# Performance work log

Hardware: AMD Instinct MI355X
Metric: run time of the kernel (lower is better)

The kernel has to match this reference:

```python
import jax, jax.numpy as jnp
import numpy as np

B, H_IN, H_OUT, SEQ_LEN = 256, 512, 512, 512


def setup_inputs() -> dict:
    key = jax.random.key(0)
    k1, k2, k3, k4, k5 = jax.random.split(key, 5)
    s = 1.0 / np.sqrt(H_OUT)  # torch GRU init scale
    return {
        "x": jax.random.normal(k1, (B, H_IN), dtype=jnp.float32),
        "W_ih": jax.random.uniform(k2, (3 * H_OUT, H_IN), jnp.float32, -s, s),
        "W_hh": jax.random.uniform(k3, (3 * H_OUT, H_OUT), jnp.float32, -s, s),
        "b_ih": jax.random.uniform(k4, (3 * H_OUT,), jnp.float32, -s, s),
        "b_hh": jax.random.uniform(k5, (3 * H_OUT,), jnp.float32, -s, s),
        "seq_len": SEQ_LEN,
    }


def reference(x, W_ih, W_hh, b_ih, b_hh, seq_len):
    # bridge: ReLU, then the same vector is fed at every timestep, so the
    # input-to-hidden projection is computed ONCE and reused across the scan.
    xr = jax.nn.relu(x)                       # [B, H_in]
    gi = xr @ W_ih.T + b_ih                   # [B, 3*H_out], constant over time
    Hh = W_hh.shape[1]
    gi_r, gi_z, gi_n = gi[:, :Hh], gi[:, Hh:2 * Hh], gi[:, 2 * Hh:]

    h0 = jnp.zeros((x.shape[0], Hh), dtype=x.dtype)

    def step(h, _):
        gh = h @ W_hh.T + b_hh                # [B, 3*H_out]
        gh_r, gh_z, gh_n = gh[:, :Hh], gh[:, Hh:2 * Hh], gh[:, 2 * Hh:]
        r = jax.nn.sigmoid(gi_r + gh_r)
        z = jax.nn.sigmoid(gi_z + gh_z)
        n = jnp.tanh(gi_n + r * gh_n)
        h_new = (1.0 - z) * n + z * h
        return h_new, h_new

    _, hs = jax.lax.scan(step, h0, None, length=seq_len)  # [S, B, H_out]
    return jnp.transpose(hs, (1, 0, 2))                   # [B, S, H_out]
```

## Files before the change

kernel.cpp:

```cpp
#include <hip/hip_runtime.h>


typedef __attribute__((ext_vector_type(8))) short short8;
typedef __attribute__((ext_vector_type(4))) float f32x4;
typedef __attribute__((ext_vector_type(4))) unsigned int u32x4;
typedef unsigned short ushort_t;
typedef unsigned int uint_t;
typedef unsigned long long u64_t;

#define NG 16
#define NM 16
#define NB 16
#define NJ 32
#define TPB 384
#define SPIN_MAX (1u << 16)
#define ABORT_IDX 8192
#define GBUF_BASE 16384
#define GRP_U32 4096
#define BUF_U32 65536

#define ALD(P) __hip_atomic_load((P), __ATOMIC_RELAXED, __HIP_MEMORY_SCOPE_AGENT)
#define AST(P, V) __hip_atomic_store((P), (V), __ATOMIC_RELAXED, __HIP_MEMORY_SCOPE_AGENT)

__device__ __forceinline__ ushort_t bf16_rne(float f) {
  uint_t u = __float_as_uint(f);
  return (ushort_t)((u + 0x7fffu + ((u >> 16) & 1u)) >> 16);
}
__device__ __forceinline__ float bf16f(ushort_t h) {
  return __uint_as_float(((uint_t)h) << 16);
}
__device__ __forceinline__ int gRow(int rs, int m) {
  int base = m * NJ;
  if (rs < 32) return base + rs;
  if (rs < 64) return 512 + base + (rs - 32);
  return 1024 + base + (rs - 64);
}

template <bool LO>
__device__ __forceinline__ void loadW(short8* dst, const float* __restrict__ W,
                                      int tile, int m, int lane) {
  int rs = tile * 16 + (lane & 15);
  const float* p = W + (size_t)gRow(rs, m) * 512 + ((lane >> 4) << 3);
#pragma unroll
  for (int c = 0; c < 16; ++c) {
    const float* pc = p + c * 32;
    short8 o;
#pragma unroll
    for (int i = 0; i < 8; ++i) {
      float v = pc[i];
      ushort_t hi = bf16_rne(v);
      o[i] = LO ? (short)bf16_rne(v - bf16f(hi)) : (short)hi;
    }
    dst[c] = o;
  }
}

__global__ __launch_bounds__(TPB, 1) void gru_kernel(
    const float* __restrict__ x, const float* __restrict__ Wih,
    const float* __restrict__ Whh, const float* __restrict__ bih,
    const float* __restrict__ bhh, float* __restrict__ out,
    uint_t* __restrict__ wsp, int NT) {
  __shared__ __align__(16) uint_t s_pb[4096];
  __shared__ __align__(16) uint_t s_xlo[4096];
  __shared__ float s_gi[96 * 17];
  __shared__ float s_gh[96 * 17];
  __shared__ float s_hloc[NB * NJ];
  __shared__ float s_bhh[NJ];
  __shared__ int s_stop;

  const int tid = threadIdx.x;
  const int lane = tid & 63;
  const int w = tid >> 6;
  const int bid = blockIdx.x;
  const int g = bid & 15;
  const int m = bid >> 4;
  const int me = (g << 4) + m;
  if (NT <= 0) return;

  uint_t* flags = wsp;
  uint_t* gbuf = wsp + GBUF_BASE;

  for (int i = tid; i < 1024; i += TPB) {
    int b = i >> 6, k0 = (i & 63) << 3;
    const float* px = x + (size_t)(g * NB + b) * 512 + k0;
    u32x4 vh, vl;
#pragma unroll
    for (int jj = 0; jj < 4; ++jj) {
      float f0 = px[2 * jj], f1 = px[2 * jj + 1];
      f0 = f0 > 0.f ? f0 : 0.f;
      f1 = f1 > 0.f ? f1 : 0.f;
      ushort_t h0 = bf16_rne(f0), h1 = bf16_rne(f1);
      vh[jj] = (uint_t)h0 | ((uint_t)h1 << 16);
      vl[jj] = (uint_t)bf16_rne(f0 - bf16f(h0)) |
               ((uint_t)bf16_rne(f1 - bf16f(h1)) << 16);
    }
    int c = k0 >> 5, kk = k0 & 31;
    int base = c * 1024 + ((((b << 6) + (kk << 1))) ^ ((b & 7) << 4));
    *(u32x4*)((char*)s_pb + base) = vh;
    *(u32x4*)((char*)s_xlo + base) = vl;
  }
  if (tid < NJ) s_bhh[tid] = bhh[1024 + m * NJ + tid];
  if (tid == 0) s_stop = 0;
  __syncthreads();

  short8 wA[16], wB[16];
  const f32x4 vzero = {0.f, 0.f, 0.f, 0.f};
  const int bcol = lane & 15;
  const int roff = ((bcol << 6) + ((lane >> 4) << 4)) ^ ((bcol & 7) << 4);
  const char* pb = (const char*)s_pb;
  const char* pxl = (const char*)s_xlo;

  f32x4 acc0 = vzero, acc1 = vzero;
  if (w < 3) {
    loadW<false>(wA, Wih, 2 * w, m, lane);
    loadW<false>(wB, Wih, 2 * w + 1, m, lane);
    {
      f32x4 a0h = vzero, a0l = vzero, a1h = vzero, a1l = vzero;
#pragma unroll
      for (int c = 0; c < 16; ++c) {
        short8 bh = *(const short8*)(pb + c * 1024 + roff);
        short8 bl = *(const short8*)(pxl + c * 1024 + roff);
        a0h = __builtin_amdgcn_mfma_f32_16x16x32_bf16(wA[c], bh, a0h, 0, 0, 0);
        a1h = __builtin_amdgcn_mfma_f32_16x16x32_bf16(wB[c], bh, a1h, 0, 0, 0);
        a0l = __builtin_amdgcn_mfma_f32_16x16x32_bf16(wA[c], bl, a0l, 0, 0, 0);
        a1l = __builtin_amdgcn_mfma_f32_16x16x32_bf16(wB[c], bl, a1l, 0, 0, 0);
      }
      acc0 = a0h + a0l;
      acc1 = a1h + a1l;
    }
    loadW<true>(wA, Wih, 2 * w, m, lane);
    loadW<true>(wB, Wih, 2 * w + 1, m, lane);
#pragma unroll
    for (int c = 0; c < 16; ++c) {
      short8 bh = *(const short8*)(pb + c * 1024 + roff);
      acc0 = __builtin_amdgcn_mfma_f32_16x16x32_bf16(wA[c], bh, acc0, 0, 0, 0);
      acc1 = __builtin_amdgcn_mfma_f32_16x16x32_bf16(wB[c], bh, acc1, 0, 0, 0);
    }
  }
  __syncthreads();
  if (w < 3) {
    int drow = (lane >> 4) << 2;
#pragma unroll
    for (int q = 0; q < 4; ++q) {
      int rs0 = 2 * w * 16 + drow + q, rs1 = rs0 + 16;
      int g0 = gRow(rs0, m), g1 = gRow(rs1, m);
      s_gi[rs0 * 17 + bcol] = acc0[q] + bih[g0] + (rs0 < 64 ? bhh[g0] : 0.f);
      s_gi[rs1 * 17 + bcol] = acc1[q] + bih[g1] + (rs1 < 64 ? bhh[g1] : 0.f);
    }
    loadW<false>(wA, Whh, 2 * w, m, lane);
    loadW<false>(wB, Whh, 2 * w + 1, m, lane);
  }
  for (int i = tid; i < 4096; i += TPB) s_pb[i] = 0u;
  for (int i = tid; i < NB * NJ; i += TPB) s_hloc[i] = 0.f;
  __syncthreads();

  const size_t outRow = (size_t)NT * 512;
  float* outBase = out + (size_t)(g * NB) * outRow + m * NJ;

  for (int t = 0; t < NT; ++t) {
    if (w < 3) {
      f32x4 aE0 = vzero, aO0 = vzero, aE1 = vzero, aO1 = vzero;
#pragma unroll
      for (int p = 0; p < 16; p += 2) {
        short8 b0 = *(const short8*)(pb + p * 1024 + roff);
        short8 b1 = *(const short8*)(pb + (p + 1) * 1024 + roff);
        aE0 = __builtin_amdgcn_mfma_f32_16x16x32_bf16(wA[p], b0, aE0, 0, 0, 0);
        aE1 = __builtin_amdgcn_mfma_f32_16x16x32_bf16(wB[p], b0, aE1, 0, 0, 0);
        aO0 = __builtin_amdgcn_mfma_f32_16x16x32_bf16(wA[p + 1], b1, aO0, 0, 0, 0);
        aO1 = __builtin_amdgcn_mfma_f32_16x16x32_bf16(wB[p + 1], b1, aO1, 0, 0, 0);
      }
      f32x4 r0 = aE0 + aO0, r1 = aE1 + aO1;
      int drow = (lane >> 4) << 2;
#pragma unroll
      for (int q = 0; q < 4; ++q) {
        s_gh[(2 * w * 16 + drow + q) * 17 + bcol] = r0[q];
        s_gh[((2 * w + 1) * 16 + drow + q) * 17 + bcol] = r1[q];
      }
    }
    __syncthreads();

    const int et = tid - 256;
    float hn[4];
    int eb_ = 0, ej0 = 0;
    if (et >= 0) {
      int b = et >> 3, j0 = (et & 7) << 2;
      eb_ = b;
      ej0 = j0;
#pragma unroll
      for (int e = 0; e < 4; ++e) {
        int j = j0 + e;
        float pr = s_gi[j * 17 + b] + s_gh[j * 17 + b];
        float pz = s_gi[(32 + j) * 17 + b] + s_gh[(32 + j) * 17 + b];
        float r = 1.f / (1.f + __expf(-pr));
        float z = 1.f / (1.f + __expf(-pz));
        float pn =
            s_gi[(64 + j) * 17 + b] + r * (s_gh[(64 + j) * 17 + b] + s_bhh[j]);
        float n = 1.f - 2.f / (1.f + __expf(2.f * pn));
        hn[e] = n + z * (s_hloc[b * 32 + j] - n);
        s_hloc[b * 32 + j] = hn[e];
      }
      uint_t w0 = (uint_t)bf16_rne(hn[0]) | ((uint_t)bf16_rne(hn[1]) << 16);
      uint_t w1 = (uint_t)bf16_rne(hn[2]) | ((uint_t)bf16_rne(hn[3]) << 16);
      u64_t pq = (u64_t)w0 | ((u64_t)w1 << 32);
      u64_t* eb64 =
          (u64_t*)(gbuf + (size_t)((t & 1) ^ 1) * BUF_U32 + g * GRP_U32);
      __hip_atomic_store(eb64 + (m << 7) + (eb_ << 3) + (et & 7), pq,
                         __ATOMIC_RELAXED, __HIP_MEMORY_SCOPE_AGENT);
    }
    __syncthreads();

    if (tid == 256)
      AST(&flags[me << 5], (uint_t)(t + 1));
    if (et >= 0) {
      f32x4 ov = {hn[0], hn[1], hn[2], hn[3]};
      __builtin_nontemporal_store(
          ov,
          (f32x4*)(outBase + (size_t)eb_ * outRow + (size_t)t * 512 + ej0));
    }
    if (w < 4 && t + 1 < NT) {
      const uint_t tgt = (uint_t)(t + 1);
      int ok = 1;
      {
        uint_t sp = 0;
        uint_t* fp = flags + (((g << 4) + (w << 2) + (lane & 3)) << 5);
        for (;;) {
          uint_t v = tgt;
          if (lane < 4) v = ALD(fp);
          if (__all((int)(v >= tgt))) break;
          ++sp;
          uint_t ab = 0;
          if ((sp & 127u) == 0u) {
            ab = ALD(&flags[ABORT_IDX]);
            if (sp > SPIN_MAX) {
              AST(&flags[ABORT_IDX], 1u);
              ab = 1;
            }
          }
          if (__any((int)(ab != 0))) {
            if (lane == 0) s_stop = 1;
            ok = 0;
            break;
          }
          __builtin_amdgcn_s_sleep(1);
        }
      }
      if (ok) {
        const u64_t* srcq =
            (const u64_t*)(gbuf + (size_t)((t + 1) & 1) * BUF_U32 +
                           g * GRP_U32) +
            (w << 9);
#define LDI(k)                                                                 \
  __hip_atomic_load(srcq + lane + ((k) << 6), __ATOMIC_RELAXED,                \
                    __HIP_MEMORY_SCOPE_AGENT)
        u64_t q0 = LDI(0), q1 = LDI(1), q2 = LDI(2), q3 = LDI(3);
        u64_t q4 = LDI(4), q5 = LDI(5), q6 = LDI(6), q7 = LDI(7);
#undef LDI
#define STI(k, qq)                                                             \
  {                                                                            \
    uint_t qb = (uint_t)(((w << 9) + lane + ((k) << 6)) << 3);                 \
    *(u64_t*)((char*)s_pb + (qb ^ (((qb >> 6) & 7u) << 4))) = (qq);            \
  }
        STI(0, q0) STI(1, q1) STI(2, q2) STI(3, q3)
        STI(4, q4) STI(5, q5) STI(6, q6) STI(7, q7)
#undef STI
      }
    }
    __syncthreads();
    if (s_stop) break;
  }
}

extern "C" void kernel_launch(void* const* d_in, const int* in_sizes, int n_in,
                              void* d_out, int out_size, void* d_ws,
                              size_t ws_size, hipStream_t stream) {
  const float* x = (const float*)d_in[0];
  const float* Wih = (const float*)d_in[1];
  const float* Whh = (const float*)d_in[2];
  const float* bih = (const float*)d_in[3];
  const float* bhh = (const float*)d_in[4];
  float* out = (float*)d_out;
  int NT = out_size / (256 * 512);
  uint_t* wsp = (uint_t*)d_ws;
  (void)hipMemsetAsync(d_ws, 0, 65536, stream);
  hipLaunchKernelGGL(gru_kernel, dim3(NG * NM), dim3(TPB), 0, stream, x, Wih,
                     Whh, bih, bhh, out, wsp, NT);
}
```

Before: 1.162 ms.

## Publish per-wave ready flags after vmcnt wait instead of a block-wide barrier

```diff
diff --git a/kernel.cpp b/kernel.cpp
--- a/kernel.cpp
+++ b/kernel.cpp
@@ -16,11 +16,16 @@
 #define SPIN_MAX (1u << 16)
 #define ABORT_IDX 8192
 #define GBUF_BASE 16384
-#define GRP_U32 4096
-#define BUF_U32 65536
+#define PAR_U64 32768
+#define GRP_U64 2048
 
 #define ALD(P) __hip_atomic_load((P), __ATOMIC_RELAXED, __HIP_MEMORY_SCOPE_AGENT)
 #define AST(P, V) __hip_atomic_store((P), (V), __ATOMIC_RELAXED, __HIP_MEMORY_SCOPE_AGENT)
+#define VMWAIT()                                                               \
+  do {                                                                         \
+    asm volatile("s_waitcnt vmcnt(0)" ::: "memory");                           \
+    __builtin_amdgcn_sched_barrier(0);                                         \
+  } while (0)
 
 __device__ __forceinline__ ushort_t bf16_rne(float f) {
   uint_t u = __float_as_uint(f);
@@ -77,8 +82,8 @@
   const int me = (g << 4) + m;
   if (NT <= 0) return;
 
-  uint_t* flags = wsp;
-  uint_t* gbuf = wsp + GBUF_BASE;
+  uint_t* flagsu = wsp;
+  u64_t* gq = (u64_t*)(wsp + GBUF_BASE);
 
   for (int i = tid; i < 1024; i += TPB) {
     int b = i >> 6, k0 = (i & 63) << 3;
@@ -158,6 +163,7 @@
   float* outBase = out + (size_t)(g * NB) * outRow + m * NJ;
 
   for (int t = 0; t < NT; ++t) {
+    const int xpar = (t + 1) & 1;
     if (w < 3) {
       f32x4 aE0 = vzero, aO0 = vzero, aE1 = vzero, aO1 = vzero;
 #pragma unroll
@@ -180,12 +186,9 @@
     __syncthreads();
 
     const int et = tid - 256;
-    float hn[4];
-    int eb_ = 0, ej0 = 0;
     if (et >= 0) {
       int b = et >> 3, j0 = (et & 7) << 2;
-      eb_ = b;
-      ej0 = j0;
+      float hn[4];
 #pragma unroll
       for (int e = 0; e < 4; ++e) {
         int j = j0 + e;
@@ -199,40 +202,40 @@
         hn[e] = n + z * (s_hloc[b * 32 + j] - n);
         s_hloc[b * 32 + j] = hn[e];
       }
-      uint_t w0 = (uint_t)bf16_rne(hn[0]) | ((uint_t)bf16_rne(hn[1]) << 16);
-      uint_t w1 = (uint_t)bf16_rne(hn[2]) | ((uint_t)bf16_rne(hn[3]) << 16);
-      u64_t pq = (u64_t)w0 | ((u64_t)w1 << 32);
-      u64_t* eb64 =
-          (u64_t*)(gbuf + (size_t)((t & 1) ^ 1) * BUF_U32 + g * GRP_U32);
-      __hip_atomic_store(eb64 + (m << 7) + (eb_ << 3) + (et & 7), pq,
-                         __ATOMIC_RELAXED, __HIP_MEMORY_SCOPE_AGENT);
-    }
-    __syncthreads();
-
-    if (tid == 256)
-      AST(&flags[me << 5], (uint_t)(t + 1));
-    if (et >= 0) {
+      if (t + 1 < NT) {
+        uint_t d0 = (uint_t)bf16_rne(hn[0]) | ((uint_t)bf16_rne(hn[1]) << 16);
+        uint_t d1 = (uint_t)bf16_rne(hn[2]) | ((uint_t)bf16_rne(hn[3]) << 16);
+        u64_t pq = (u64_t)d0 | ((u64_t)d1 << 32);
+        u64_t* dst = gq + (size_t)xpar * PAR_U64 + g * GRP_U64 + (m << 7) +
+                     (b << 3) + (et & 7);
+        AST(dst, pq);
+        VMWAIT();
+        if (lane == 0)
+          AST(&flagsu[(me << 5) + ((w - 4) << 3)], (uint_t)(t + 1));
+      }
       f32x4 ov = {hn[0], hn[1], hn[2], hn[3]};
       __builtin_nontemporal_store(
-          ov,
-          (f32x4*)(outBase + (size_t)eb_ * outRow + (size_t)t * 512 + ej0));
-    }
+          ov, (f32x4*)(outBase + (size_t)b * outRow + (size_t)t * 512 + j0));
+    }
+
     if (w < 4 && t + 1 < NT) {
       const uint_t tgt = (uint_t)(t + 1);
       int ok = 1;
       {
         uint_t sp = 0;
-        uint_t* fp = flags + (((g << 4) + (w << 2) + (lane & 3)) << 5);
+        uint_t* fp = flagsu +
+                     ((((g << 4) + (w << 2) + (lane >> 1)) << 5) +
+                      ((lane & 1) << 3));
         for (;;) {
           uint_t v = tgt;
-          if (lane < 4) v = ALD(fp);
+          if (lane < 8) v = ALD(fp);
           if (__all((int)(v >= tgt))) break;
           ++sp;
           uint_t ab = 0;
           if ((sp & 127u) == 0u) {
-            ab = ALD(&flags[ABORT_IDX]);
+            ab = ALD(&flagsu[ABORT_IDX]);
             if (sp > SPIN_MAX) {
-              AST(&flags[ABORT_IDX], 1u);
+              AST(&flagsu[ABORT_IDX], 1u);
               ab = 1;
             }
           }
@@ -246,12 +249,8 @@
       }
       if (ok) {
         const u64_t* srcq =
-            (const u64_t*)(gbuf + (size_t)((t + 1) & 1) * BUF_U32 +
-                           g * GRP_U32) +
-            (w << 9);
-#define LDI(k)                                                                 \
-  __hip_atomic_load(srcq + lane + ((k) << 6), __ATOMIC_RELAXED,                \
-                    __HIP_MEMORY_SCOPE_AGENT)
+            gq + (size_t)xpar * PAR_U64 + g * GRP_U64 + (w << 9);
+#define LDI(k) ALD(srcq + lane + ((k) << 6))
         u64_t q0 = LDI(0), q1 = LDI(1), q2 = LDI(2), q3 = LDI(3);
         u64_t q4 = LDI(4), q5 = LDI(5), q6 = LDI(6), q7 = LDI(7);
 #undef LDI
```

Measured after the change: 1.391 ms. 1.2x slower.
